# Performance work log

Hardware: AMD Instinct MI355X
Metric: run time of the kernel (lower is better)

## Reference

```python
import jax, jax.numpy as jnp
import numpy as np

WH, WW = 7, 7
SH, SW = 3, 3
NUM_HEADS = 8


def _rel_pos_index(wh, ww):
    coords = np.stack(np.meshgrid(np.arange(wh), np.arange(ww), indexing='ij')).reshape(2, -1)
    rel = (coords[:, :, None] - coords[:, None, :]).transpose(1, 2, 0)  # [N,N,2]
    rel[..., 0] += wh - 1
    rel[..., 1] += ww - 1
    rel[..., 0] *= 2 * ww - 1
    return rel.sum(-1)  # [N,N] int


def _attn_mask(Hp, Wp, wh, ww, sh, sw):
    img = np.zeros((Hp, Wp), dtype=np.float32)
    cnt = 0
    for hs in (slice(0, -wh), slice(-wh, -sh), slice(-sh, None)):
        for ws in (slice(0, -ww), slice(-ww, -sw), slice(-sw, None)):
            img[hs, ws] = cnt
            cnt += 1
    win = img.reshape(Hp // wh, wh, Wp // ww, ww).transpose(0, 2, 1, 3).reshape(-1, wh * ww)  # [nW,N]
    diff = win[:, None, :] - win[:, :, None]  # [nW,N,N]
    return np.where(diff != 0, -100.0, 0.0).astype(np.float32)


def _layernorm(x, g, b, eps=1e-5):
    mu = jnp.mean(x, -1, keepdims=True)
    var = jnp.mean(jnp.square(x - mu), -1, keepdims=True)
    return (x - mu) * jax.lax.rsqrt(var + eps) * g + b


def setup_inputs() -> dict:
    key = jax.random.key(0)
    ks = jax.random.split(key, 12)
    B, H, W, C = 32, 56, 56, 256
    hid = 4 * C
    s = lambda k, *shape: jax.random.normal(k, shape, jnp.float32) * 0.02
    return {
        'x': jax.random.normal(ks[0], (B, H * W, C), jnp.float32),
        'g1': jnp.ones((C,), jnp.float32), 'b1': jnp.zeros((C,), jnp.float32),
        'qkv_w': s(ks[1], 3 * C, C), 'qkv_b': jnp.zeros((3 * C,), jnp.float32),
        'bias_table': s(ks[2], (2 * WH - 1) * (2 * WW - 1), NUM_HEADS),
        'proj_w': s(ks[3], C, C), 'proj_b': jnp.zeros((C,), jnp.float32),
        'g2': jnp.ones((C,), jnp.float32), 'b2': jnp.zeros((C,), jnp.float32),
        'w1': s(ks[4], hid, C), 'bm1': jnp.zeros((hid,), jnp.float32),
        'w2': s(ks[5], C, hid), 'bm2': jnp.zeros((C,), jnp.float32),
        'H': H, 'W': W,
    }


def reference(x, g1, b1, qkv_w, qkv_b, bias_table, proj_w, proj_b, g2, b2, w1, bm1, w2, bm2, H, W):
    B, L, C = x.shape
    wh, ww = WH, WW
    nH = NUM_HEADS
    hd = C // nH
    scale = hd ** -0.5
    N = wh * ww

    shortcut = x
    h = _layernorm(x, g1, b1).reshape(B, H, W, C)
    pad_b = (wh - H % wh) % wh
    pad_r = (ww - W % ww) % ww
    if pad_b or pad_r:
        h = jnp.pad(h, ((0, 0), (0, pad_b), (0, pad_r), (0, 0)))
    Hp, Wp = h.shape[1], h.shape[2]

    h = jnp.roll(h, (-SH, -SW), axis=(1, 2))
    # window partition -> [B*nW, N, C]
    nWh, nWw = Hp // wh, Wp // ww
    xw = h.reshape(B, nWh, wh, nWw, ww, C).transpose(0, 1, 3, 2, 4, 5).reshape(-1, N, C)

    qkv = jnp.einsum('bnc,oc->bno', xw, qkv_w) + qkv_b  # [B*nW, N, 3C]
    qkv = qkv.reshape(-1, N, 3, nH, hd).transpose(2, 0, 3, 1, 4)
    q, k, v = qkv[0] * scale, qkv[1], qkv[2]  # [B*nW, nH, N, hd]
    attn = jnp.einsum('whnd,whmd->whnm', q, k)  # [B*nW, nH, N, N]

    rpi = jnp.asarray(_rel_pos_index(wh, ww))
    bias = bias_table[rpi.reshape(-1)].reshape(N, N, nH).transpose(2, 0, 1)  # [nH,N,N]
    attn = attn + bias[None]

    mask = jnp.asarray(_attn_mask(Hp, Wp, wh, ww, SH, SW))  # [nW,N,N]
    nW = mask.shape[0]
    attn = attn.reshape(B, nW, nH, N, N) + mask[None, :, None]
    attn = jax.nn.softmax(attn.reshape(-1, nH, N, N), axis=-1)

    out = jnp.einsum('whnm,whmd->whnd', attn, v).transpose(0, 2, 1, 3).reshape(-1, N, C)
    out = jnp.einsum('bnc,oc->bno', out, proj_w) + proj_b

    # window reverse
    out = out.reshape(B, nWh, nWw, wh, ww, C).transpose(0, 1, 3, 2, 4, 5).reshape(B, Hp, Wp, C)
    out = jnp.roll(out, (SH, SW), axis=(1, 2))
    if pad_b or pad_r:
        out = out[:, :H, :W, :]
    out = out.reshape(B, H * W, C)

    x = shortcut + out
    m = _layernorm(x, g2, b2)
    m = jax.nn.gelu(jnp.einsum('blc,oc->blo', m, w1) + bm1, approximate=False)
    m = jnp.einsum('blh,oh->blo', m, w2) + bm2
    return x + m
```

## Files before the change

### kernel.cpp

```cpp
#include <hip/hip_runtime.h>
#include <hip/hip_bf16.h>

#define DEVI __device__ __forceinline__

typedef short bf16x8 __attribute__((ext_vector_type(8)));
typedef float f32x4  __attribute__((ext_vector_type(4)));

constexpr int MROWS = 100352;
constexpr int BM = 128, BN = 128, BK = 64;

DEVI int win_row_to_token(int r) {
  int b   = r / 3136;
  int rem = r - b * 3136;
  int wi  = rem / 49;
  int t   = rem - wi * 49;
  int nwh = wi >> 3, nww = wi & 7;
  int th = t / 7, tw = t - th * 7;
  int h = nwh * 7 + th + 3; if (h >= 56) h -= 56;
  int w = nww * 7 + tw + 3; if (w >= 56) w -= 56;
  return b * 3136 + h * 56 + w;
}

DEVI unsigned short f2bf(float f) {
  __hip_bfloat16 h = __float2bfloat16(f);
  return __builtin_bit_cast(unsigned short, h);
}

__global__ void cvt_kernel(const float* __restrict__ in, __hip_bfloat16* __restrict__ out, int n) {
  int i = blockIdx.x * 256 + threadIdx.x;
  if (i < n) out[i] = __float2bfloat16(in[i]);
}

template<bool WIN>
__global__ __launch_bounds__(256) void ln_kernel(
    const float* __restrict__ xin, const float* __restrict__ g,
    const float* __restrict__ b, __hip_bfloat16* __restrict__ outb)
{
  int r = blockIdx.x * 4 + (threadIdx.x >> 6);
  int l = threadIdx.x & 63;
  int tok = WIN ? win_row_to_token(r) : r;
  float4 xv = *(const float4*)&xin[(size_t)tok * 256 + l * 4];
  float s = xv.x + xv.y + xv.z + xv.w;
  float q = xv.x * xv.x + xv.y * xv.y + xv.z * xv.z + xv.w * xv.w;
  #pragma unroll
  for (int off = 32; off; off >>= 1) { s += __shfl_xor(s, off); q += __shfl_xor(q, off); }
  float mu = s * (1.0f / 256.0f);
  float var = q * (1.0f / 256.0f) - mu * mu;
  float rs = rsqrtf(var + 1e-5f);
  float4 gv = *(const float4*)&g[l * 4];
  float4 bv = *(const float4*)&b[l * 4];
  ushort4 st;
  st.x = f2bf((xv.x - mu) * rs * gv.x + bv.x);
  st.y = f2bf((xv.y - mu) * rs * gv.y + bv.y);
  st.z = f2bf((xv.z - mu) * rs * gv.z + bv.z);
  st.w = f2bf((xv.w - mu) * rs * gv.w + bv.w);
  *(ushort4*)&outb[(size_t)r * 256 + l * 4] = st;
}

enum { EPI_QKV = 0, EPI_PROJ = 1, EPI_MLP1 = 2, EPI_MLP2 = 3 };

template<int EPI>
__global__ __launch_bounds__(256) void gemm_kernel(
    const __hip_bfloat16* __restrict__ A,
    const __hip_bfloat16* __restrict__ Bw,
    int N, int K,
    const float* __restrict__ bias,
    const float* __restrict__ xres,
    float* __restrict__ outf,
    __hip_bfloat16* __restrict__ outb)
{
  __shared__ __align__(16) __hip_bfloat16 lsA[BM * BK];
  __shared__ __align__(16) __hip_bfloat16 lsB[BN * BK];
  const int ntiles = N / BN;
  int mt = blockIdx.x / ntiles;
  int nt = blockIdx.x - mt * ntiles;
  const int w = threadIdx.x >> 6, l = threadIdx.x & 63;
  const int wr = (w >> 1) * 64, wc = (w & 1) * 64;
  f32x4 acc[4][4] = {};
  const __hip_bfloat16* Abase = A  + (size_t)mt * BM * K;
  const __hip_bfloat16* Bbase = Bw + (size_t)nt * BN * K;
  const int srow = l >> 3;
  const int skb  = (l & 7) * 8;

  for (int kt = 0; kt < K; kt += BK) {
    #pragma unroll
    for (int i = 0; i < 4; ++i) {
      int chunk = w * 4 + i;
      int row = chunk * 8 + srow;
      __builtin_amdgcn_global_load_lds(
          (const __attribute__((address_space(1))) void*)(Abase + (size_t)row * K + kt + skb),
          (__attribute__((address_space(3))) void*)(&lsA[chunk * 512]), 16, 0, 0);
      __builtin_amdgcn_global_load_lds(
          (const __attribute__((address_space(1))) void*)(Bbase + (size_t)row * K + kt + skb),
          (__attribute__((address_space(3))) void*)(&lsB[chunk * 512]), 16, 0, 0);
    }
    __syncthreads();
    #pragma unroll
    for (int kk = 0; kk < 2; ++kk) {
      bf16x8 af[4], bfr[4];
      #pragma unroll
      for (int mi = 0; mi < 4; ++mi)
        af[mi] = *(const bf16x8*)&lsA[(wr + mi * 16 + (l & 15)) * 64 + kk * 32 + (l >> 4) * 8];
      #pragma unroll
      for (int ni = 0; ni < 4; ++ni)
        bfr[ni] = *(const bf16x8*)&lsB[(wc + ni * 16 + (l & 15)) * 64 + kk * 32 + (l >> 4) * 8];
      #pragma unroll
      for (int mi = 0; mi < 4; ++mi)
        #pragma unroll
        for (int ni = 0; ni < 4; ++ni)
          acc[mi][ni] = __builtin_amdgcn_mfma_f32_16x16x32_bf16(af[mi], bfr[ni], acc[mi][ni], 0, 0, 0);
    }
    __syncthreads();
  }

  const int lcol = l & 15, lrow4 = (l >> 4) * 4;
  #pragma unroll
  for (int mi = 0; mi < 4; ++mi) {
    #pragma unroll
    for (int j = 0; j < 4; ++j) {
      int grow = mt * BM + wr + mi * 16 + lrow4 + j;
      int orow = grow;
      if (EPI == EPI_PROJ) orow = win_row_to_token(grow);
      #pragma unroll
      for (int ni = 0; ni < 4; ++ni) {
        int gcol = nt * BN + wc + ni * 16 + lcol;
        float v = acc[mi][ni][j] + bias[gcol];
        if (EPI == EPI_QKV) {
          outb[(size_t)grow * 768 + gcol] = __float2bfloat16(v);
        } else if (EPI == EPI_PROJ) {
          size_t o = (size_t)orow * 256 + gcol;
          outf[o] = xres[o] + v;
        } else if (EPI == EPI_MLP1) {
          float ge = 0.5f * v * (1.0f + erff(v * 0.70710678118654752f));
          outb[(size_t)grow * 1024 + gcol] = __float2bfloat16(ge);
        } else {
          size_t o = (size_t)grow * 256 + gcol;
          outf[o] += v;
        }
      }
    }
  }
}

__global__ __launch_bounds__(256) void bias_prep_kernel(
    const float* __restrict__ bt, float* __restrict__ Sadd)
{
  int blk = blockIdx.x;
  int cls = blk >> 3, h = blk & 7;
  int re = cls >> 1, ce = cls & 1;
  int lane = threadIdx.x & 63, fs = threadIdx.x >> 6;
  int g = lane >> 4, lm = lane & 15;
  #pragma unroll
  for (int i = 0; i < 4; ++i) {
    int f = fs * 4 + i;
    int mi = f >> 2, ni = f & 3;
    int key = ni * 16 + lm;
    f32x4 v;
    #pragma unroll
    for (int j = 0; j < 4; ++j) {
      int q = mi * 16 + g * 4 + j;
      float val;
      if (key >= 49) {
        val = -1e30f;
      } else {
        int qq = q > 48 ? 48 : q;
        int qh = qq / 7, qw = qq - qh * 7;
        int kh = key / 7, kw = key - kh * 7;
        int rpi = (qh - kh + 6) * 13 + (qw - kw + 6);
        val = bt[rpi * 8 + h];
        int rq = (re ? (qh < 4 ? 1 : 2) : 0) * 3 + (ce ? (qw < 4 ? 1 : 2) : 0);
        int rk = (re ? (kh < 4 ? 1 : 2) : 0) * 3 + (ce ? (kw < 4 ? 1 : 2) : 0);
        if (rq != rk) val -= 100.0f;
      }
      v[j] = val;
    }
    ((f32x4*)Sadd)[(blk * 16 + f) * 64 + lane] = v;
  }
}

__global__ __launch_bounds__(256) void attn_mfma_kernel(
    const __hip_bfloat16* __restrict__ qkv,
    const float* __restrict__ Sadd,
    __hip_bfloat16* __restrict__ attn_out)
{
  __shared__ __align__(16) __hip_bfloat16 Pl[4][64 * 72];
  int blk = blockIdx.x;
  int win = blk >> 1, half = blk & 1;
  int w = threadIdx.x >> 6, l = threadIdx.x & 63;
  int head = half * 4 + w;
  int g = l >> 4, lm = l & 15;
  int wi = win & 63;
  int cls = (((wi >> 3) == 7) ? 2 : 0) | (((wi & 7) == 7) ? 1 : 0);
  const __hip_bfloat16* base = qkv + (size_t)win * 49 * 768 + head * 32;

  bf16x8 aQ[4], bK[4];
  #pragma unroll
  for (int mi = 0; mi < 4; ++mi) {
    int q = mi * 16 + lm; if (q > 48) q = 48;
    aQ[mi] = *(const bf16x8*)(base + q * 768 + g * 8);
  }
  #pragma unroll
  for (int ni = 0; ni < 4; ++ni) {
    int k = ni * 16 + lm; if (k > 48) k = 48;
    bK[ni] = *(const bf16x8*)(base + 256 + k * 768 + g * 8);
  }
  f32x4 acc[4][4] = {};
  #pragma unroll
  for (int mi = 0; mi < 4; ++mi)
    #pragma unroll
    for (int ni = 0; ni < 4; ++ni)
      acc[mi][ni] = __builtin_amdgcn_mfma_f32_16x16x32_bf16(aQ[mi], bK[ni], acc[mi][ni], 0, 0, 0);

  const float scale = 0.17677669529663687f;
  const f32x4* Sb = (const f32x4*)Sadd + (size_t)(cls * 8 + head) * 16 * 64 + l;

  f32x4 rsum[4];
  __hip_bfloat16* P = Pl[w];
  #pragma unroll
  for (int mi = 0; mi < 4; ++mi) {
    #pragma unroll
    for (int ni = 0; ni < 4; ++ni) {
      f32x4 sv = Sb[(mi * 4 + ni) * 64];
      #pragma unroll
      for (int j = 0; j < 4; ++j) acc[mi][ni][j] = acc[mi][ni][j] * scale + sv[j];
    }
    f32x4 mx = acc[mi][0];
    #pragma unroll
    for (int ni = 1; ni < 4; ++ni)
      #pragma unroll
      for (int j = 0; j < 4; ++j) mx[j] = fmaxf(mx[j], acc[mi][ni][j]);
    #pragma unroll
    for (int msk = 1; msk < 16; msk <<= 1)
      #pragma unroll
      for (int j = 0; j < 4; ++j) mx[j] = fmaxf(mx[j], __shfl_xor(mx[j], msk));
    f32x4 sm = {};
    #pragma unroll
    for (int ni = 0; ni < 4; ++ni)
      #pragma unroll
      for (int j = 0; j < 4; ++j) {
        float e = __expf(acc[mi][ni][j] - mx[j]);
        acc[mi][ni][j] = e;
        sm[j] += e;
      }
    #pragma unroll
    for (int msk = 1; msk < 16; msk <<= 1)
      #pragma unroll
      for (int j = 0; j < 4; ++j) sm[j] += __shfl_xor(sm[j], msk);
    rsum[mi] = sm;
    #pragma unroll
    for (int ni = 0; ni < 4; ++ni)
      #pragma unroll
      for (int j = 0; j < 4; ++j) {
        int q = mi * 16 + g * 4 + j;
        int key = ni * 16 + lm;
        P[q * 72 + key] = __float2bfloat16(acc[mi][ni][j]);
      }
  }

  bf16x8 bV[2][2];
  #pragma unroll
  for (int s = 0; s < 2; ++s)
    #pragma unroll
    for (int n2 = 0; n2 < 2; ++n2) {
      bf16x8 vv;
      #pragma unroll
      for (int e = 0; e < 8; ++e) {
        int key = s * 32 + g * 8 + e; if (key > 48) key = 48;
        vv[e] = __builtin_bit_cast(short, base[512 + key * 768 + n2 * 16 + lm]);
      }
      bV[s][n2] = vv;
    }

  f32x4 o[4][2] = {};
  #pragma unroll
  for (int s = 0; s < 2; ++s)
    #pragma unroll
    for (int mi2 = 0; mi2 < 4; ++mi2) {
      bf16x8 aP = *(const bf16x8*)&P[(mi2 * 16 + lm) * 72 + s * 32 + g * 8];
      #pragma unroll
      for (int n2 = 0; n2 < 2; ++n2)
        o[mi2][n2] = __builtin_amdgcn_mfma_f32_16x16x32_bf16(aP, bV[s][n2], o[mi2][n2], 0, 0, 0);
    }

  #pragma unroll
  for (int mi2 = 0; mi2 < 4; ++mi2) {
    f32x4 li;
    #pragma unroll
    for (int j = 0; j < 4; ++j) li[j] = 1.0f / rsum[mi2][j];
    #pragma unroll
    for (int n2 = 0; n2 < 2; ++n2)
      #pragma unroll
      for (int j = 0; j < 4; ++j) {
        int q = mi2 * 16 + g * 4 + j;
        if (q < 49)
          attn_out[((size_t)win * 49 + q) * 256 + head * 32 + n2 * 16 + lm] =
              __float2bfloat16(o[mi2][n2][j] * li[j]);
      }
  }
}

extern "C" void kernel_launch(void* const* d_in, const int* in_sizes, int n_in,
                              void* d_out, int out_size, void* d_ws, size_t ws_size,
                              hipStream_t stream) {
  const float* x          = (const float*)d_in[0];
  const float* g1         = (const float*)d_in[1];
  const float* b1         = (const float*)d_in[2];
  const float* qkv_w      = (const float*)d_in[3];
  const float* qkv_b      = (const float*)d_in[4];
  const float* bias_table = (const float*)d_in[5];
  const float* proj_w     = (const float*)d_in[6];
  const float* proj_b     = (const float*)d_in[7];
  const float* g2         = (const float*)d_in[8];
  const float* b2         = (const float*)d_in[9];
  const float* w1         = (const float*)d_in[10];
  const float* bm1        = (const float*)d_in[11];
  const float* w2         = (const float*)d_in[12];
  const float* bm2        = (const float*)d_in[13];
  float* out = (float*)d_out;

  char* ws = (char*)d_ws;
  __hip_bfloat16* A_ln   = (__hip_bfloat16*)(ws);
  __hip_bfloat16* qkvb   = (__hip_bfloat16*)(ws + 51380224);
  __hip_bfloat16* attn_o = (__hip_bfloat16*)(ws + 205520896);
  __hip_bfloat16* hidden = qkvb;
  __hip_bfloat16* qkv_wb  = (__hip_bfloat16*)(ws + 256901120);
  __hip_bfloat16* proj_wb = qkv_wb + 196608;
  __hip_bfloat16* w1b     = proj_wb + 65536;
  __hip_bfloat16* w2b     = w1b + 262144;
  float* Sadd = (float*)(ws + 258473984);

  cvt_kernel<<<(196608 + 255) / 256, 256, 0, stream>>>(qkv_w, qkv_wb, 196608);
  cvt_kernel<<<(65536  + 255) / 256, 256, 0, stream>>>(proj_w, proj_wb, 65536);
  cvt_kernel<<<(262144 + 255) / 256, 256, 0, stream>>>(w1, w1b, 262144);
  cvt_kernel<<<(262144 + 255) / 256, 256, 0, stream>>>(w2, w2b, 262144);
  bias_prep_kernel<<<32, 256, 0, stream>>>(bias_table, Sadd);

  ln_kernel<true><<<MROWS / 4, 256, 0, stream>>>(x, g1, b1, A_ln);

  gemm_kernel<EPI_QKV><<<(MROWS / BM) * (768 / BN), 256, 0, stream>>>(
      A_ln, qkv_wb, 768, 256, qkv_b, nullptr, nullptr, qkvb);

  attn_mfma_kernel<<<4096, 256, 0, stream>>>(qkvb, Sadd, attn_o);

  gemm_kernel<EPI_PROJ><<<(MROWS / BM) * (256 / BN), 256, 0, stream>>>(
      attn_o, proj_wb, 256, 256, proj_b, x, out, nullptr);

  ln_kernel<false><<<MROWS / 4, 256, 0, stream>>>(out, g2, b2, A_ln);

  gemm_kernel<EPI_MLP1><<<(MROWS / BM) * (1024 / BN), 256, 0, stream>>>(
      A_ln, w1b, 1024, 256, bm1, nullptr, nullptr, hidden);

  gemm_kernel<EPI_MLP2><<<(MROWS / BM) * (256 / BN), 256, 0, stream>>>(
      hidden, w2b, 256, 1024, bm2, nullptr, out, nullptr);
}
```

Baseline: 560.8 us.

## Add persistent strip GEMM with register-resident weights for K=256 GEMMs

Adds a persistent 512-thread GEMM kernel for the three K=256 GEMMs (QKV, proj, MLP1). Each block walks a contiguous range of (n-tile, m-tile) pairs within one XCD's slice of rows. It keeps the 128-column weight strip in registers across m-tiles and double-buffers swizzled A tiles into LDS with direct global-to-LDS loads. The old GEMM also gets an XCD-aware block swizzle, which now only affects MLP2. The aim is to cut repeated weight loads and launch and tail overhead, at the cost of high register pressure (128 VGPRs of B fragments plus accumulators) and a fixed 256-block grid.

```diff
diff --git a/kernel.cpp b/kernel.cpp
--- a/kernel.cpp
+++ b/kernel.cpp
@@ -58,6 +58,136 @@
 }
 
 enum { EPI_QKV = 0, EPI_PROJ = 1, EPI_MLP1 = 2, EPI_MLP2 = 3 };
+
+template<int EPI>
+__global__ __launch_bounds__(512, 2) void strip_gemm(
+    const __hip_bfloat16* __restrict__ A,
+    const __hip_bfloat16* __restrict__ Bw,
+    int ntiles,
+    const float* __restrict__ bias,
+    const float* __restrict__ xres,
+    float* __restrict__ outf,
+    __hip_bfloat16* __restrict__ outb)
+{
+  constexpr int K = 256;
+  __shared__ __align__(16) __hip_bfloat16 Al[2][256 * 64];
+
+  const int tid = threadIdx.x;
+  const int w = tid >> 6, l = tid & 63;
+  const int wr = w >> 1, wc = w & 1;
+  const int g = l >> 4, lm = l & 15;
+
+  const int b   = blockIdx.x;
+  const int xcd = b & 7;
+  const int cu  = b >> 3;
+  const int T   = 49 * ntiles;
+  const int t0  = (cu * T) >> 5;
+  const int t1  = ((cu + 1) * T) >> 5;
+
+  auto issue = [&](int mt, int c, int p) {
+    const __hip_bfloat16* Ab = A + (size_t)mt * 256 * K + c * 64;
+    #pragma unroll
+    for (int j = 0; j < 4; ++j) {
+      int row = j * 64 + w * 8 + (l >> 3);
+      int u = (l & 7) ^ (row & 7);
+      __builtin_amdgcn_global_load_lds(
+          (const __attribute__((address_space(1))) void*)((const char*)(Ab + (size_t)row * K) + u * 16),
+          (__attribute__((address_space(3))) void*)(&Al[p][(j * 512 + w * 64) * 8]),
+          16, 0, 0);
+    }
+  };
+
+  bf16x8 Bf[4][8];
+  f32x4  acc[4][4];
+  int cur_nt = -1;
+  int p = 0;
+
+  {
+    int mt0 = xcd * 49 + (t0 % 49);
+    issue(mt0, 0, 0);
+  }
+
+  for (int t = t0; t < t1; ++t) {
+    int nt = t / 49;
+    int mt = xcd * 49 + (t - nt * 49);
+
+    if (nt != cur_nt) {
+      #pragma unroll
+      for (int ni = 0; ni < 4; ++ni)
+        #pragma unroll
+        for (int kf = 0; kf < 8; ++kf)
+          Bf[ni][kf] = *(const bf16x8*)&Bw[
+              (size_t)(nt * 128 + wc * 64 + ni * 16 + lm) * K + kf * 32 + g * 8];
+      cur_nt = nt;
+    }
+    #pragma unroll
+    for (int mi = 0; mi < 4; ++mi)
+      #pragma unroll
+      for (int ni = 0; ni < 4; ++ni)
+        acc[mi][ni] = f32x4{0.f, 0.f, 0.f, 0.f};
+
+    #pragma unroll
+    for (int c = 0; c < 4; ++c) {
+      bool lastc = (t == t1 - 1) && (c == 3);
+      if (!lastc) {
+        int tn = (c < 3) ? t : t + 1;
+        int cn = (c < 3) ? c + 1 : 0;
+        int ntn = tn / 49;
+        int mtn = xcd * 49 + (tn - ntn * 49);
+        issue(mtn, cn, p ^ 1);
+        asm volatile("s_waitcnt vmcnt(4)" ::: "memory");
+      } else {
+        asm volatile("s_waitcnt vmcnt(0)" ::: "memory");
+      }
+      __builtin_amdgcn_s_barrier();
+      asm volatile("" ::: "memory");
+
+      #pragma unroll
+      for (int kk = 0; kk < 2; ++kk) {
+        bf16x8 af[4];
+        #pragma unroll
+        for (int mi = 0; mi < 4; ++mi) {
+          int r = wr * 64 + mi * 16 + lm;
+          int u = (kk * 4 + g) ^ (r & 7);
+          af[mi] = *(const bf16x8*)&Al[p][r * 64 + u * 8];
+        }
+        #pragma unroll
+        for (int mi = 0; mi < 4; ++mi)
+          #pragma unroll
+          for (int ni = 0; ni < 4; ++ni)
+            acc[mi][ni] = __builtin_amdgcn_mfma_f32_16x16x32_bf16(
+                af[mi], Bf[ni][c * 2 + kk], acc[mi][ni], 0, 0, 0);
+      }
+
+      asm volatile("" ::: "memory");
+      __builtin_amdgcn_s_barrier();
+      p ^= 1;
+    }
+
+    #pragma unroll
+    for (int mi = 0; mi < 4; ++mi)
+      #pragma unroll
+      for (int j = 0; j < 4; ++j) {
+        int grow = mt * 256 + wr * 64 + mi * 16 + g * 4 + j;
+        int orow = grow;
+        if (EPI == EPI_PROJ) orow = win_row_to_token(grow);
+        #pragma unroll
+        for (int ni = 0; ni < 4; ++ni) {
+          int gcol = nt * 128 + wc * 64 + ni * 16 + lm;
+          float v = acc[mi][ni][j] + bias[gcol];
+          if (EPI == EPI_QKV) {
+            outb[(size_t)grow * 768 + gcol] = __float2bfloat16(v);
+          } else if (EPI == EPI_PROJ) {
+            size_t o = (size_t)orow * 256 + gcol;
+            outf[o] = xres[o] + v;
+          } else {
+            float ge = 0.5f * v * (1.0f + erff(v * 0.70710678118654752f));
+            outb[(size_t)grow * 1024 + gcol] = __float2bfloat16(ge);
+          }
+        }
+      }
+  }
+}
 
 template<int EPI>
 __global__ __launch_bounds__(256) void gemm_kernel(
@@ -72,8 +202,11 @@
   __shared__ __align__(16) __hip_bfloat16 lsA[BM * BK];
   __shared__ __align__(16) __hip_bfloat16 lsB[BN * BK];
   const int ntiles = N / BN;
-  int mt = blockIdx.x / ntiles;
-  int nt = blockIdx.x - mt * ntiles;
+  int bswz = blockIdx.x;
+  int nwg = gridDim.x;
+  if ((nwg & 7) == 0) bswz = (blockIdx.x & 7) * (nwg >> 3) + (blockIdx.x >> 3);
+  int mt = bswz / ntiles;
+  int nt = bswz - mt * ntiles;
   const int w = threadIdx.x >> 6, l = threadIdx.x & 63;
   const int wr = (w >> 1) * 64, wc = (w & 1) * 64;
   f32x4 acc[4][4] = {};
@@ -337,18 +470,18 @@
 
   ln_kernel<true><<<MROWS / 4, 256, 0, stream>>>(x, g1, b1, A_ln);
 
-  gemm_kernel<EPI_QKV><<<(MROWS / BM) * (768 / BN), 256, 0, stream>>>(
-      A_ln, qkv_wb, 768, 256, qkv_b, nullptr, nullptr, qkvb);
+  strip_gemm<EPI_QKV><<<256, 512, 0, stream>>>(
+      A_ln, qkv_wb, 6, qkv_b, nullptr, nullptr, qkvb);
 
   attn_mfma_kernel<<<4096, 256, 0, stream>>>(qkvb, Sadd, attn_o);
 
-  gemm_kernel<EPI_PROJ><<<(MROWS / BM) * (256 / BN), 256, 0, stream>>>(
-      attn_o, proj_wb, 256, 256, proj_b, x, out, nullptr);
+  strip_gemm<EPI_PROJ><<<256, 512, 0, stream>>>(
+      attn_o, proj_wb, 2, proj_b, x, out, nullptr);
 
   ln_kernel<false><<<MROWS / 4, 256, 0, stream>>>(out, g2, b2, A_ln);
 
-  gemm_kernel<EPI_MLP1><<<(MROWS / BM) * (1024 / BN), 256, 0, stream>>>(
-      A_ln, w1b, 1024, 256, bm1, nullptr, nullptr, hidden);
+  strip_gemm<EPI_MLP1><<<256, 512, 0, stream>>>(
+      A_ln, w1b, 8, bm1, nullptr, nullptr, hidden);
 
   gemm_kernel<EPI_MLP2><<<(MROWS / BM) * (256 / BN), 256, 0, stream>>>(
       hidden, w2b, 256, 1024, bm2, nullptr, out, nullptr);
```

Result: slower. 599.9 us (+7.0%).

## Replace tiled GEMMs with persistent strip GEMM keeping weights in registers

Applied to the files above, without the earlier changes.

The per-tile GEMM is replaced by a persistent kernel launched with 256 blocks of 512 threads. Each block walks a contiguous range of (M-tile, N-tile, K-block) work items assigned per XCD. Weight fragments stay in registers across consecutive M tiles, and A tiles stream through a swizzled triple-buffered LDS pipeline with explicit vmcnt waits and barriers. The aim is to cut repeated B loads, LDS bank conflicts and launch overhead, and to overlap loads with MFMA. The cost is heavy register pressure (Bf alone is 128 VGPRs) at one block per CU, plus fragile hand-written synchronisation.

```diff
diff --git a/kernel.cpp b/kernel.cpp
--- a/kernel.cpp
+++ b/kernel.cpp
@@ -7,7 +7,6 @@
 typedef float f32x4  __attribute__((ext_vector_type(4)));
 
 constexpr int MROWS = 100352;
-constexpr int BM = 128, BN = 128, BK = 64;
 
 DEVI int win_row_to_token(int r) {
   int b   = r / 3136;
@@ -59,85 +58,141 @@
 
 enum { EPI_QKV = 0, EPI_PROJ = 1, EPI_MLP1 = 2, EPI_MLP2 = 3 };
 
-template<int EPI>
-__global__ __launch_bounds__(256) void gemm_kernel(
+template<int EPI, int KTOT>
+__global__ __launch_bounds__(512, 1) void strip_gemm(
     const __hip_bfloat16* __restrict__ A,
     const __hip_bfloat16* __restrict__ Bw,
-    int N, int K,
+    int ntiles,
     const float* __restrict__ bias,
     const float* __restrict__ xres,
     float* __restrict__ outf,
     __hip_bfloat16* __restrict__ outb)
 {
-  __shared__ __align__(16) __hip_bfloat16 lsA[BM * BK];
-  __shared__ __align__(16) __hip_bfloat16 lsB[BN * BK];
-  const int ntiles = N / BN;
-  int mt = blockIdx.x / ntiles;
-  int nt = blockIdx.x - mt * ntiles;
-  const int w = threadIdx.x >> 6, l = threadIdx.x & 63;
-  const int wr = (w >> 1) * 64, wc = (w & 1) * 64;
-  f32x4 acc[4][4] = {};
-  const __hip_bfloat16* Abase = A  + (size_t)mt * BM * K;
-  const __hip_bfloat16* Bbase = Bw + (size_t)nt * BN * K;
-  const int srow = l >> 3;
-  const int skb  = (l & 7) * 8;
-
-  for (int kt = 0; kt < K; kt += BK) {
-    #pragma unroll
-    for (int i = 0; i < 4; ++i) {
-      int chunk = w * 4 + i;
-      int row = chunk * 8 + srow;
+  constexpr int NKB = KTOT / 256;
+  __shared__ __align__(16) __hip_bfloat16 Al[3][256 * 64];
+
+  const int tid = threadIdx.x;
+  const int w = tid >> 6, l = tid & 63;
+  const int wr = w >> 1, wc = w & 1;
+  const int g = l >> 4, lm = l & 15;
+
+  const int b   = blockIdx.x;
+  const int xcd = b & 7;
+  const int cu  = b >> 3;
+  const int T   = 49 * ntiles;
+  const int t0  = (cu * T) >> 5;
+  const int t1  = ((cu + 1) * T) >> 5;
+  const int nquads = (t1 - t0) * NKB;
+
+  auto issue = [&](int mt, int koff, int buf) {
+    const __hip_bfloat16* Ab = A + (size_t)mt * 256 * KTOT + koff;
+    #pragma unroll
+    for (int j = 0; j < 4; ++j) {
+      int row = j * 64 + w * 8 + (l >> 3);
+      int u = (l & 7) ^ (row & 7);
       __builtin_amdgcn_global_load_lds(
-          (const __attribute__((address_space(1))) void*)(Abase + (size_t)row * K + kt + skb),
-          (__attribute__((address_space(3))) void*)(&lsA[chunk * 512]), 16, 0, 0);
-      __builtin_amdgcn_global_load_lds(
-          (const __attribute__((address_space(1))) void*)(Bbase + (size_t)row * K + kt + skb),
-          (__attribute__((address_space(3))) void*)(&lsB[chunk * 512]), 16, 0, 0);
-    }
-    __syncthreads();
-    #pragma unroll
-    for (int kk = 0; kk < 2; ++kk) {
-      bf16x8 af[4], bfr[4];
-      #pragma unroll
-      for (int mi = 0; mi < 4; ++mi)
-        af[mi] = *(const bf16x8*)&lsA[(wr + mi * 16 + (l & 15)) * 64 + kk * 32 + (l >> 4) * 8];
+          (const __attribute__((address_space(1))) void*)((const char*)(Ab + (size_t)row * KTOT) + u * 16),
+          (__attribute__((address_space(3))) void*)(&Al[buf][j * 4096 + w * 512]),
+          16, 0, 0);
+    }
+  };
+
+  bf16x8 Bf[4][8];
+  f32x4  acc[4][4];
+  int cur_key = -1;
+  int p = 0;
+
+  issue(xcd * 49 + (t0 - (t0 / 49) * 49), 0, 0);
+
+  for (int qd = 0; qd < nquads; ++qd) {
+    int tt = t0 + qd / NKB;
+    int kb = qd - (qd / NKB) * NKB;
+    int nt = tt / 49;
+    int mt = xcd * 49 + (tt - nt * 49);
+
+    int key = nt * NKB + kb;
+    if (key != cur_key) {
       #pragma unroll
       for (int ni = 0; ni < 4; ++ni)
-        bfr[ni] = *(const bf16x8*)&lsB[(wc + ni * 16 + (l & 15)) * 64 + kk * 32 + (l >> 4) * 8];
+        #pragma unroll
+        for (int kf = 0; kf < 8; ++kf)
+          Bf[ni][kf] = *(const bf16x8*)&Bw[
+              (size_t)(nt * 128 + wc * 64 + ni * 16 + lm) * KTOT + kb * 256 + kf * 32 + g * 8];
+      cur_key = key;
+    }
+    if (kb == 0) {
       #pragma unroll
       for (int mi = 0; mi < 4; ++mi)
         #pragma unroll
         for (int ni = 0; ni < 4; ++ni)
-          acc[mi][ni] = __builtin_amdgcn_mfma_f32_16x16x32_bf16(af[mi], bfr[ni], acc[mi][ni], 0, 0, 0);
-    }
-    __syncthreads();
-  }
-
-  const int lcol = l & 15, lrow4 = (l >> 4) * 4;
-  #pragma unroll
-  for (int mi = 0; mi < 4; ++mi) {
-    #pragma unroll
-    for (int j = 0; j < 4; ++j) {
-      int grow = mt * BM + wr + mi * 16 + lrow4 + j;
-      int orow = grow;
-      if (EPI == EPI_PROJ) orow = win_row_to_token(grow);
-      #pragma unroll
-      for (int ni = 0; ni < 4; ++ni) {
-        int gcol = nt * BN + wc + ni * 16 + lcol;
-        float v = acc[mi][ni][j] + bias[gcol];
-        if (EPI == EPI_QKV) {
-          outb[(size_t)grow * 768 + gcol] = __float2bfloat16(v);
-        } else if (EPI == EPI_PROJ) {
-          size_t o = (size_t)orow * 256 + gcol;
-          outf[o] = xres[o] + v;
-        } else if (EPI == EPI_MLP1) {
-          float ge = 0.5f * v * (1.0f + erff(v * 0.70710678118654752f));
-          outb[(size_t)grow * 1024 + gcol] = __float2bfloat16(ge);
-        } else {
-          size_t o = (size_t)grow * 256 + gcol;
-          outf[o] += v;
+          acc[mi][ni] = f32x4{0.f, 0.f, 0.f, 0.f};
+    }
+
+    #pragma unroll
+    for (int c = 0; c < 4; ++c) {
+      int np = (p == 2) ? 0 : p + 1;
+      bool last = (qd == nquads - 1) && (c == 3);
+      if (!last) {
+        int qn = (c < 3) ? qd : qd + 1;
+        int cn = (c < 3) ? c + 1 : 0;
+        int tn  = t0 + qn / NKB;
+        int kbn = qn - (qn / NKB) * NKB;
+        int ntn = tn / 49;
+        int mtn = xcd * 49 + (tn - ntn * 49);
+        issue(mtn, kbn * 256 + cn * 64, np);
+        asm volatile("s_waitcnt vmcnt(4)" ::: "memory");
+      } else {
+        asm volatile("s_waitcnt vmcnt(0)" ::: "memory");
+      }
+      __builtin_amdgcn_s_barrier();
+      asm volatile("" ::: "memory");
+
+      #pragma unroll
+      for (int kk = 0; kk < 2; ++kk) {
+        bf16x8 af[4];
+        #pragma unroll
+        for (int mi = 0; mi < 4; ++mi) {
+          int r = wr * 64 + mi * 16 + lm;
+          int u = (kk * 4 + g) ^ (r & 7);
+          af[mi] = *(const bf16x8*)&Al[p][r * 64 + u * 8];
         }
-      }
+        #pragma unroll
+        for (int mi = 0; mi < 4; ++mi)
+          #pragma unroll
+          for (int ni = 0; ni < 4; ++ni)
+            acc[mi][ni] = __builtin_amdgcn_mfma_f32_16x16x32_bf16(
+                af[mi], Bf[ni][c * 2 + kk], acc[mi][ni], 0, 0, 0);
+      }
+      asm volatile("" ::: "memory");
+      p = np;
+    }
+
+    if (kb == NKB - 1) {
+      #pragma unroll
+      for (int mi = 0; mi < 4; ++mi)
+        #pragma unroll
+        for (int j = 0; j < 4; ++j) {
+          int grow = mt * 256 + wr * 64 + mi * 16 + g * 4 + j;
+          int orow = grow;
+          if (EPI == EPI_PROJ) orow = win_row_to_token(grow);
+          #pragma unroll
+          for (int ni = 0; ni < 4; ++ni) {
+            int gcol = nt * 128 + wc * 64 + ni * 16 + lm;
+            float v = acc[mi][ni][j] + bias[gcol];
+            if (EPI == EPI_QKV) {
+              outb[(size_t)grow * 768 + gcol] = __float2bfloat16(v);
+            } else if (EPI == EPI_PROJ) {
+              size_t o = (size_t)orow * 256 + gcol;
+              outf[o] = xres[o] + v;
+            } else if (EPI == EPI_MLP1) {
+              float ge = 0.5f * v * (1.0f + erff(v * 0.70710678118654752f));
+              outb[(size_t)grow * 1024 + gcol] = __float2bfloat16(ge);
+            } else {
+              size_t o = (size_t)grow * 256 + gcol;
+              outf[o] += v;
+            }
+          }
+        }
     }
   }
 }
@@ -337,19 +392,19 @@
 
   ln_kernel<true><<<MROWS / 4, 256, 0, stream>>>(x, g1, b1, A_ln);
 
-  gemm_kernel<EPI_QKV><<<(MROWS / BM) * (768 / BN), 256, 0, stream>>>(
-      A_ln, qkv_wb, 768, 256, qkv_b, nullptr, nullptr, qkvb);
+  strip_gemm<EPI_QKV, 256><<<256, 512, 0, stream>>>(
+      A_ln, qkv_wb, 6, qkv_b, nullptr, nullptr, qkvb);
 
   attn_mfma_kernel<<<4096, 256, 0, stream>>>(qkvb, Sadd, attn_o);
 
-  gemm_kernel<EPI_PROJ><<<(MROWS / BM) * (256 / BN), 256, 0, stream>>>(
-      attn_o, proj_wb, 256, 256, proj_b, x, out, nullptr);
+  strip_gemm<EPI_PROJ, 256><<<256, 512, 0, stream>>>(
+      attn_o, proj_wb, 2, proj_b, x, out, nullptr);
 
   ln_kernel<false><<<MROWS / 4, 256, 0, stream>>>(out, g2, b2, A_ln);
 
-  gemm_kernel<EPI_MLP1><<<(MROWS / BM) * (1024 / BN), 256, 0, stream>>>(
-      A_ln, w1b, 1024, 256, bm1, nullptr, nullptr, hidden);
-
-  gemm_kernel<EPI_MLP2><<<(MROWS / BM) * (256 / BN), 256, 0, stream>>>(
-      hidden, w2b, 256, 1024, bm2, nullptr, out, nullptr);
-}
+  strip_gemm<EPI_MLP1, 256><<<256, 512, 0, stream>>>(
+      A_ln, w1b, 8, bm1, nullptr, nullptr, hidden);
+
+  strip_gemm<EPI_MLP2, 1024><<<256, 512, 0, stream>>>(
+      hidden, w2b, 2, bm2, nullptr, out, nullptr);
+}
```

New measurement: 712.8 us. +27.1%, slower.
